# Optimization experiments

Hardware: AMD Instinct MI355X
Metric: run time of the kernel (lower is better)

The kernel has to match this reference:

```python
import jax, jax.numpy as jnp
from jax import lax
import numpy as np

V, D, H, E, L, B = 512, 128, 64, 4, 60, 4096
ADJ = 184  # ((180 + 7) // 8) * 8


def setup_inputs() -> dict:
    key = jax.random.key(0)
    it = iter(jax.random.split(key, 64))

    def nrm(shape, s=0.05):
        return jax.random.normal(next(it), shape, dtype=jnp.float32) * s

    x = jax.random.randint(next(it), (B, L), 0, V, dtype=jnp.int32)
    inp = {"x": x, "emb": nrm((V, D), 0.02).at[0].set(0.0)}  # padding_idx=0 row zero
    for d in ("f", "r"):
        inp[f"w_ih_{d}"] = nrm((4 * H, D)); inp[f"w_hh_{d}"] = nrm((4 * H, H))
        inp[f"b_ih_{d}"] = nrm((4 * H,)); inp[f"b_hh_{d}"] = nrm((4 * H,))
    for p, i_, h_, o_ in (("e", 1, 16, 8), ("l", 1, 16, 8), ("c", V, 32, 16), ("p", 6, 24, 12), ("x", 4, 16, 8)):
        inp[f"{p}_w1"] = nrm((h_, i_)); inp[f"{p}_b1"] = nrm((h_,))
        inp[f"{p}_w2"] = nrm((o_, h_)); inp[f"{p}_b2"] = nrm((o_,))
    inp["fp_w"] = nrm((ADJ, 180)); inp["fp_b"] = nrm((ADJ,))
    inp["attn_w"] = nrm((3 * ADJ, ADJ)); inp["attn_b"] = nrm((3 * ADJ,))
    inp["out_w"] = nrm((ADJ, ADJ)); inp["out_b"] = nrm((ADJ,))
    for i, (o_, i_) in enumerate(((128, ADJ), (64, 128), (32, 64), (E, 32)), 1):
        inp[f"g_w{i}"] = nrm((o_, i_)); inp[f"g_b{i}"] = nrm((o_,))
    return inp


def _mlp2(h, w1, b1, w2, b2):
    return jnp.maximum(h @ w1.T + b1, 0.0) @ w2.T + b2


def _lstm_final(xe, w_ih, w_hh, b_ih, b_hh):
    # torch LSTM gate order i, f, g, o; returns final hidden state [B, H]
    xg = jnp.einsum('bld,gd->blg', xe, w_ih) + b_ih
    h0 = jnp.zeros((xe.shape[0], H), xe.dtype)

    def step(carry, g_t):
        h, c = carry
        g = g_t + h @ w_hh.T + b_hh
        i, f, gg, o = jnp.split(g, 4, axis=-1)
        c = jax.nn.sigmoid(f) * c + jax.nn.sigmoid(i) * jnp.tanh(gg)
        h = jax.nn.sigmoid(o) * jnp.tanh(c)
        return (h, c), None

    (h, _), _ = lax.scan(step, (h0, h0), jnp.swapaxes(xg, 0, 1))
    return h


def _sequence_stats(x):
    # Fully vectorized equivalent of the per-sequence python loops
    f32 = jnp.float32
    mask = x != 0
    vlen = mask.sum(1)                                       # [B]
    vlenf = jnp.maximum(vlen, 1).astype(f32)
    pos = jnp.arange(L)
    # per-row histogram over valid tokens (torch.bincount of valid_seq)
    counts = jnp.zeros((B, V), f32).at[jnp.arange(B)[:, None], x].add(mask.astype(f32))
    probs = counts / jnp.maximum(counts.sum(1, keepdims=True), 1.0)
    entropy = -jnp.sum(probs * jnp.log(probs + 1e-8), axis=1)
    entropy = jnp.where(vlen > 1, entropy, 0.0)
    char_dist = counts / vlenf[:, None]
    # compact valid tokens to the front (torch: seq[seq != 0]), stable argsort
    order = jnp.argsort((~mask).astype(jnp.int32), axis=1)
    cseq = jnp.take_along_axis(x, order, axis=1)
    cseq = jnp.where(pos[None] < vlen[:, None], cseq, 0)
    a, b = cseq[:, :-1], cseq[:, 1:]
    pairmask = pos[: L - 1][None] < (vlen - 1)[:, None]
    den1 = jnp.maximum(vlen - 1, 1).astype(f32)
    repeat = ((a == b) & pairmask).sum(1) / den1
    inc = ((b > a) & pairmask).sum(1) / den1
    dec = ((b < a) & pairmask).sum(1) / den1
    m2 = pos[: L - 2][None] < (vlen - 2)[:, None]
    per = ((cseq[:, :-2] == cseq[:, 2:]) & m2).sum(1) / jnp.maximum(vlen - 2, 1)
    per = jnp.where(vlen >= 4, per, 0.0)
    diversity = (counts > 0).sum(1) / vlenf
    # longest run of equal consecutive tokens via cummax of reset positions
    eq = jnp.concatenate([jnp.zeros((B, 1), bool), (cseq[:, 1:] == cseq[:, :-1]) & (pos[1:][None] < vlen[:, None])], 1)
    lastreset = lax.cummax(jnp.where(eq, -1, pos[None]), axis=1)
    runlen = pos[None] - lastreset + 1
    max_rep = jnp.where(pos[None] < vlen[:, None], runlen, 0).max(1) / vlenf
    pattern = jnp.stack([repeat, inc, dec, per, diversity, max_rep], 1).astype(f32)
    pattern = jnp.where((vlen > 1)[:, None], pattern, 0.0)
    # unique bigrams: sort pair codes, count distinct valid codes
    codes = jnp.where(pairmask, a * V + b, -1)
    s = jnp.sort(codes, axis=1)
    prevc = jnp.concatenate([jnp.full((B, 1), -2, s.dtype), s[:, :-1]], 1)
    comp_ratio = ((s != prevc) & (s >= 0)).sum(1) / den1
    info_density = entropy / jnp.log(jnp.maximum(vlen, 2).astype(f32))
    # local complexity: mean over sliding windows of (#unique / w), w = min(5, len//2)
    wsel = jnp.minimum(5, vlen // 2)
    local = jnp.zeros((B,), f32)
    for w in (2, 3, 4, 5):
        nwin = L - w + 1
        sh = [cseq[:, k:k + nwin] for k in range(w)]
        u = jnp.ones((B, nwin), f32)
        for k in range(1, w):
            isnew = jnp.ones((B, nwin), bool)
            for m in range(k):
                isnew = isnew & (sh[k] != sh[m])
            u = u + isnew
        winmask = pos[:nwin][None] < (vlen - w + 1)[:, None]
        lc = (u * winmask).sum(1) / w / jnp.maximum(vlen - w + 1, 1)
        local = jnp.where(wsel == w, lc, local)
    trans = 1.0 - repeat  # transitions/(len-1) == 1 - repeat_ratio
    complexity = jnp.stack([comp_ratio, info_density, local, trans], 1).astype(f32)
    complexity = jnp.where((vlen > 1)[:, None], complexity, 0.0)
    return entropy, vlen, char_dist, pattern, complexity


def reference(x, emb, w_ih_f, w_hh_f, b_ih_f, b_hh_f, w_ih_r, w_hh_r, b_ih_r, b_hh_r, e_w1, e_b1, e_w2, e_b2, l_w1, l_b1, l_w2, l_b2, c_w1, c_b1, c_w2, c_b2, p_w1, p_b1, p_w2, p_b2, x_w1, x_b1, x_w2, x_b2, fp_w, fp_b, attn_w, attn_b, out_w, out_b, g_w1, g_b1, g_w2, g_b2, g_w3, g_b3, g_w4, g_b4):
    entropy, vlen, char_dist, pattern, complexity = _sequence_stats(x)
    xe = emb[x]                                               # [B, L, D]
    h_f = _lstm_final(xe, w_ih_f, w_hh_f, b_ih_f, b_hh_f)
    h_r = _lstm_final(xe[:, ::-1], w_ih_r, w_hh_r, b_ih_r, b_hh_r)
    feats = jnp.concatenate([
        h_f, h_r,
        _mlp2((entropy / 4.0)[:, None], e_w1, e_b1, e_w2, e_b2),
        _mlp2((vlen.astype(jnp.float32) / 60.0)[:, None], l_w1, l_b1, l_w2, l_b2),
        _mlp2(char_dist, c_w1, c_b1, c_w2, c_b2),
        _mlp2(pattern, p_w1, p_b1, p_w2, p_b2),
        _mlp2(complexity, x_w1, x_b1, x_w2, x_b2),
    ], axis=1)                                                # [B, 180]
    f = feats @ fp_w.T + fp_b                                 # [B, 184]
    # MultiheadAttention with seq_len == 1: softmax over a single key is 1,
    # so attended = out_proj(v_proj(f)) exactly (q/k projections cancel).
    wv, bv = attn_w[2 * ADJ:], attn_b[2 * ADJ:]
    attended = (f @ wv.T + bv) @ out_w.T + out_b
    h = jnp.maximum(attended @ g_w1.T + g_b1, 0.0)
    h = jnp.maximum(h @ g_w2.T + g_b2, 0.0)
    h = jnp.maximum(h @ g_w3.T + g_b3, 0.0)
    logits = h @ g_w4.T + g_b4
    return jax.nn.softmax(logits, axis=-1)  # eval path (training=False)
```

## Files before the change

### kernel.cpp

```cpp
#include <hip/hip_runtime.h>

#define BATCH 4096
#define SEQL  60
#define VOC   512
#define EMBD  128
#define HID   64
#define GATES 256
#define ADJ   184

typedef __attribute__((ext_vector_type(8))) short short8;
typedef __attribute__((ext_vector_type(4))) float f32x4;

__device__ __forceinline__ float sigm(float x) {
  return __builtin_amdgcn_rcpf(1.f + __expf(-x));
}
__device__ __forceinline__ float tanh_(float x) {
  float e = __expf(2.f * x);
  return 1.f - 2.f * __builtin_amdgcn_rcpf(e + 1.f);
}
__device__ __forceinline__ unsigned short f2bf(float f) {
  unsigned int u = __float_as_uint(f);
  unsigned int r = (u + 0x7fffu + ((u >> 16) & 1u)) >> 16;
  return (unsigned short)r;
}
__device__ __forceinline__ float dot4(float4 a, float4 b, float acc) {
  acc = fmaf(a.x, b.x, acc); acc = fmaf(a.y, b.y, acc);
  acc = fmaf(a.z, b.z, acc); acc = fmaf(a.w, b.w, acc);
  return acc;
}
__device__ __forceinline__ float wsumf(float v) {
  #pragma unroll
  for (int s = 32; s > 0; s >>= 1) v += __shfl_xor(v, s, 64);
  return v;
}
__device__ __forceinline__ int wsumi(int v) {
  #pragma unroll
  for (int s = 32; s > 0; s >>= 1) v += __shfl_xor(v, s, 64);
  return v;
}
__device__ __forceinline__ int wmaxi(int v) {
  #pragma unroll
  for (int s = 32; s > 0; s >>= 1) v = max(v, __shfl_xor(v, s, 64));
  return v;
}

__global__ __launch_bounds__(256) void k_mega(
    const int* __restrict__ x, const float* __restrict__ emb,
    const float* __restrict__ wih_f, const float* __restrict__ bif, const float* __restrict__ bhf,
    const float* __restrict__ wih_r, const float* __restrict__ bir, const float* __restrict__ bhr,
    const float* __restrict__ whh_f, const float* __restrict__ whh_r,
    const float* __restrict__ g_w1, const float* __restrict__ g_b1,
    const float* __restrict__ out_w, const float* __restrict__ out_b,
    const float* __restrict__ attn_w, const float* __restrict__ attn_b,
    const float* __restrict__ fp_w, const float* __restrict__ fp_b,
    const float* __restrict__ g_w2, const float* __restrict__ g_w3,
    const float* __restrict__ g_w4,
    float* __restrict__ ent_o, float* __restrict__ vlen_o,
    float* __restrict__ pat_o, float* __restrict__ cpx_o,
    unsigned int* __restrict__ cnt_o,
    float* __restrict__ G_f, float* __restrict__ G_r,
    unsigned short* __restrict__ Wfrag,
    float* __restrict__ A, float* __restrict__ avb,
    float* __restrict__ Bp, float* __restrict__ vb,
    float* __restrict__ g_w2t, float* __restrict__ g_w3t, float* __restrict__ g_w4t) {
  __shared__ unsigned int cnt[4][512];
  __shared__ unsigned short q[4][68];
  const int bid = blockIdx.x;
  const int tid = threadIdx.x;

  if (bid < 1024) {
    const int lane = tid & 63;
    const int wid = tid >> 6;
    const int row = bid * 4 + wid;
    unsigned int* cr = cnt[wid];
    unsigned short* qr = q[wid];

    for (int i = lane; i < 512; i += 64) cr[i] = 0u;
    qr[lane] = 0;
    if (lane < 4) qr[64 + lane] = 0;
    int v = (lane < 60) ? x[row * 60 + lane] : 0;
    bool act = (v != 0);
    unsigned long long amask = __ballot(act);
    int n = __popcll(amask);
    __syncthreads();
    if (act) {
      int pos = __popcll(amask & ((1ull << lane) - 1ull));
      qr[pos] = (unsigned short)v;
      atomicAdd(&cr[v], 1u);
    }
    __syncthreads();

    float vlenf = (float)(n >= 1 ? n : 1);
    float inv = 1.f / vlenf;

    float ent = 0.f; int distinct = 0;
    #pragma unroll
    for (int j = 0; j < 8; j++) {
      unsigned int c = cr[lane + j * 64];
      if (c) {
        distinct++;
        float p = (float)c * inv;
        ent -= p * __logf(p + 1e-8f);
      }
    }
    ent = wsumf(ent);
    distinct = wsumi(distinct);

    int a = qr[lane], b = qr[lane + 1], c2 = qr[lane + 2];
    bool v1 = (lane + 1 < n);
    bool v2 = (lane + 2 < n);
    int rep  = __popcll(__ballot(v1 && (a == b)));
    int incs = __popcll(__ballot(v1 && (b > a)));
    int decs = __popcll(__ballot(v1 && (b < a)));
    int per2 = __popcll(__ballot(v2 && (a == c2)));

    int prev = (lane > 0) ? (int)qr[lane - 1] : -1;
    bool isst = (lane < n) && (lane == 0 || a != prev);
    unsigned long long smask = __ballot(isst);
    int len = 0;
    if (isst) {
      unsigned long long hi = (lane < 63) ? (smask >> (lane + 1)) : 0ull;
      int next = hi ? (lane + __ffsll((unsigned long long)hi)) : n;
      len = next - lane;
    }
    int maxrun = wmaxi(len);

    int unique = 1;
    int lim = v1 ? lane : 0;
    for (int jj = 0; jj < lim; jj++) {
      if ((int)qr[jj] == a && (int)qr[jj + 1] == b) { unique = 0; break; }
    }
    int dc = __popcll(__ballot(v1 && unique));

    int wl = n >> 1; if (wl > 5) wl = 5;
    float local = 0.f;
    if (wl >= 2) {
      bool pv = (lane + wl <= n);
      int u = 0;
      if (pv) {
        int t0 = qr[lane], t1 = qr[lane + 1], t2 = qr[lane + 2];
        int t3 = qr[lane + 3], t4 = qr[lane + 4];
        u = 1;
        u += (t1 != t0);
        if (wl >= 3) u += (int)((t2 != t1) && (t2 != t0));
        if (wl >= 4) u += (int)((t3 != t2) && (t3 != t1) && (t3 != t0));
        if (wl >= 5) u += (int)((t4 != t3) && (t4 != t2) && (t4 != t1) && (t4 != t0));
      }
      int usum = wsumi(u);
      int denw = n - wl + 1; if (denw < 1) denw = 1;
      local = (float)usum / (float)wl / (float)denw;
    }

    float den1 = (float)((n - 1) >= 1 ? (n - 1) : 1);
    float repeat = (float)rep / den1;
    float per = (n >= 4) ? (float)per2 / (float)((n - 2) >= 1 ? (n - 2) : 1) : 0.f;
    float entz = (n > 1) ? ent : 0.f;
    float z = (n > 1) ? 1.f : 0.f;

    if (lane == 0) {
      ent_o[row] = entz;
      vlen_o[row] = (float)n;
      pat_o[row * 6 + 0] = repeat * z;
      pat_o[row * 6 + 1] = (float)incs / den1 * z;
      pat_o[row * 6 + 2] = (float)decs / den1 * z;
      pat_o[row * 6 + 3] = per * z;
      pat_o[row * 6 + 4] = (float)distinct * inv * z;
      pat_o[row * 6 + 5] = (float)maxrun * inv * z;
      cpx_o[row * 4 + 0] = (float)dc / den1 * z;
      cpx_o[row * 4 + 1] = entz / __logf((float)(n >= 2 ? n : 2)) * z;
      cpx_o[row * 4 + 2] = local * z;
      cpx_o[row * 4 + 3] = (1.f - repeat) * z;
    }
    for (int i = lane; i < 128; i += 64) {
      unsigned int p = cr[4 * i] | (cr[4 * i + 1] << 8) |
                       (cr[4 * i + 2] << 16) | (cr[4 * i + 3] << 24);
      cnt_o[row * 128 + i] = p;
    }
  } else if (bid < 1152) {
    const int bx = bid - 1024;
    const int dir = bx >> 6;
    const int rem = bx & 63;
    const int v0 = (rem >> 2) * 32;
    const int j0 = (rem & 3) * 64;
    const float* W = dir ? wih_r : wih_f;
    const float* bi = dir ? bir : bif;
    const float* bh = dir ? bhr : bhf;
    float* G = dir ? G_r : G_f;
    const int vp = tid >> 4;
    const int jq = tid & 15;
    const int v = v0 + vp * 2;
    const int j = j0 + jq * 4;
    const int gg = j >> 6;
    const int u0 = j & 63;

    const float4* E0 = (const float4*)(emb + (size_t)v * 128);
    const float4* E1 = (const float4*)(emb + (size_t)(v + 1) * 128);
    const float4* W0 = (const float4*)(W + (size_t)j * 128);
    const float4* W1 = (const float4*)(W + (size_t)(j + 1) * 128);
    const float4* W2 = (const float4*)(W + (size_t)(j + 2) * 128);
    const float4* W3 = (const float4*)(W + (size_t)(j + 3) * 128);

    float a00 = 0.f, a01 = 0.f, a02 = 0.f, a03 = 0.f;
    float a10 = 0.f, a11 = 0.f, a12 = 0.f, a13 = 0.f;
    #pragma unroll 4
    for (int d4 = 0; d4 < 32; d4++) {
      float4 e0 = E0[d4], e1 = E1[d4];
      float4 w0 = W0[d4], w1 = W1[d4], w2 = W2[d4], w3 = W3[d4];
      a00 = dot4(e0, w0, a00); a01 = dot4(e0, w1, a01);
      a02 = dot4(e0, w2, a02); a03 = dot4(e0, w3, a03);
      a10 = dot4(e1, w0, a10); a11 = dot4(e1, w1, a11);
      a12 = dot4(e1, w2, a12); a13 = dot4(e1, w3, a13);
    }
    float b0v = bi[j] + bh[j], b1v = bi[j + 1] + bh[j + 1];
    float b2v = bi[j + 2] + bh[j + 2], b3v = bi[j + 3] + bh[j + 3];
    float* g0 = G + (size_t)v * 256 + u0 * 4 + gg;
    g0[0]  = a00 + b0v; g0[4]  = a01 + b1v;
    g0[8]  = a02 + b2v; g0[12] = a03 + b3v;
    float* g1 = g0 + 256;
    g1[0]  = a10 + b0v; g1[4]  = a11 + b1v;
    g1[8]  = a12 + b2v; g1[12] = a13 + b3v;
  } else if (bid < 1280) {
    const int i = bid - 1152;
    const int j = tid;
    const float* g1r = g_w1 + (size_t)i * ADJ;
    if (j < ADJ) {
      float a0 = 0.f, a1 = 0.f, a2 = 0.f, a3 = 0.f;
      for (int k = 0; k < ADJ; k += 4) {
        a0 = fmaf(g1r[k],     out_w[(size_t)(k)     * ADJ + j], a0);
        a1 = fmaf(g1r[k + 1], out_w[(size_t)(k + 1) * ADJ + j], a1);
        a2 = fmaf(g1r[k + 2], out_w[(size_t)(k + 2) * ADJ + j], a2);
        a3 = fmaf(g1r[k + 3], out_w[(size_t)(k + 3) * ADJ + j], a3);
      }
      A[(size_t)i * ADJ + j] = (a0 + a1) + (a2 + a3);
    } else if (j == ADJ) {
      float a0 = 0.f;
      for (int k = 0; k < ADJ; k++) a0 = fmaf(g1r[k], out_b[k], a0);
      avb[i] = a0 + g_b1[i];
    }
  } else if (bid < 1464) {
    const int k = bid - 1280;
    const int j = tid;
    const float* wvr = attn_w + (size_t)(2 * ADJ + k) * ADJ;
    if (j < 180) {
      float a0 = 0.f, a1 = 0.f, a2 = 0.f, a3 = 0.f;
      for (int m = 0; m < ADJ; m += 4) {
        a0 = fmaf(wvr[m],     fp_w[(size_t)(m)     * 180 + j], a0);
        a1 = fmaf(wvr[m + 1], fp_w[(size_t)(m + 1) * 180 + j], a1);
        a2 = fmaf(wvr[m + 2], fp_w[(size_t)(m + 2) * 180 + j], a2);
        a3 = fmaf(wvr[m + 3], fp_w[(size_t)(m + 3) * 180 + j], a3);
      }
      Bp[(size_t)k * 180 + j] = (a0 + a1) + (a2 + a3);
    } else if (j == 180) {
      float a0 = 0.f;
      for (int m = 0; m < ADJ; m++) a0 = fmaf(wvr[m], fp_b[m], a0);
      vb[k] = a0 + attn_b[2 * ADJ + k];
    }
  } else if (bid < 1480) {
    const int id = (bid - 1464) * 256 + tid;
    const int lane = id & 63;
    const int fc = id >> 6;
    const int c = fc & 1;
    const int gg = (fc >> 1) & 3;
    const int w = (fc >> 3) & 3;
    const int dir = fc >> 5;
    const float* whh = dir ? whh_r : whh_f;
    const int n = gg * 64 + w * 16 + (lane & 15);
    const int kb = c * 32 + (lane >> 4) * 8;
    unsigned short* o = Wfrag + (size_t)id * 8;
    #pragma unroll
    for (int j = 0; j < 8; j++) o[j] = f2bf(whh[n * 64 + kb + j]);
  } else {
    for (int i = tid; i < 64 * 128; i += 256) {
      int o = i >> 7, k = i & 127;
      g_w2t[k * 64 + o] = g_w2[i];
    }
    for (int i = tid; i < 32 * 64; i += 256) {
      int o = i >> 6, k = i & 63;
      g_w3t[k * 32 + o] = g_w3[i];
    }
    if (tid < 128) {
      int o = tid >> 5, k = tid & 31;
      g_w4t[k * 4 + o] = g_w4[tid];
    }
  }
}

__global__ __launch_bounds__(192) void k_prep2(
    const float* __restrict__ A, const float* __restrict__ avb,
    const float* __restrict__ Bp, const float* __restrict__ vb,
    float* __restrict__ C1t, float* __restrict__ c1b) {
  const int i = blockIdx.x, j = threadIdx.x;
  const float* Ar = A + (size_t)i * ADJ;
  if (j < 180) {
    float a0 = 0.f, a1 = 0.f, a2 = 0.f, a3 = 0.f;
    for (int k = 0; k < ADJ; k += 4) {
      a0 = fmaf(Ar[k],     Bp[(size_t)(k)     * 180 + j], a0);
      a1 = fmaf(Ar[k + 1], Bp[(size_t)(k + 1) * 180 + j], a1);
      a2 = fmaf(Ar[k + 2], Bp[(size_t)(k + 2) * 180 + j], a2);
      a3 = fmaf(Ar[k + 3], Bp[(size_t)(k + 3) * 180 + j], a3);
    }
    C1t[(size_t)j * 128 + i] = (a0 + a1) + (a2 + a3);
  } else if (j == 180) {
    float a0 = 0.f;
    for (int k = 0; k < ADJ; k++) a0 = fmaf(Ar[k], vb[k], a0);
    c1b[i] = a0 + avb[i];
  }
}

#define LSTM_STEP(T, CUR, NXT)                                                 \
  {                                                                            \
    const unsigned short* hb = hbuf[(T) & 1];                                  \
    short8 a0 = *(const short8*)(hb + ln * 72 + kg * 8);                       \
    short8 a1 = *(const short8*)(hb + ln * 72 + 32 + kg * 8);                  \
    if ((T) < 59) {                                                            \
      int tsn = dir ? (58 - (T)) : ((T) + 1);                                  \
      unsigned long long tp =                                                  \
          *(const unsigned long long*)(tokp + tsn * 16 + kg * 4);              \
      int ta = (int)(tp & 0xffffull), tb = (int)((tp >> 16) & 0xffffull);      \
      int tc = (int)((tp >> 32) & 0xffffull), td = (int)(tp >> 48);            \
      NXT[0] = *(const float4*)(G + (size_t)ta * 256 + u4);                    \
      NXT[1] = *(const float4*)(G + (size_t)tb * 256 + u4);                    \
      NXT[2] = *(const float4*)(G + (size_t)tc * 256 + u4);                    \
      NXT[3] = *(const float4*)(G + (size_t)td * 256 + u4);                    \
    }                                                                          \
    f32x4 z0 = {0.f, 0.f, 0.f, 0.f};                                           \
    f32x4 acc0 = z0, acc1 = z0, acc2 = z0, acc3 = z0;                          \
    acc0 = __builtin_amdgcn_mfma_f32_16x16x32_bf16(a0, bfr[0][0], acc0, 0, 0, 0); \
    acc1 = __builtin_amdgcn_mfma_f32_16x16x32_bf16(a0, bfr[1][0], acc1, 0, 0, 0); \
    acc2 = __builtin_amdgcn_mfma_f32_16x16x32_bf16(a0, bfr[2][0], acc2, 0, 0, 0); \
    acc3 = __builtin_amdgcn_mfma_f32_16x16x32_bf16(a0, bfr[3][0], acc3, 0, 0, 0); \
    acc0 = __builtin_amdgcn_mfma_f32_16x16x32_bf16(a1, bfr[0][1], acc0, 0, 0, 0); \
    acc1 = __builtin_amdgcn_mfma_f32_16x16x32_bf16(a1, bfr[1][1], acc1, 0, 0, 0); \
    acc2 = __builtin_amdgcn_mfma_f32_16x16x32_bf16(a1, bfr[2][1], acc2, 0, 0, 0); \
    acc3 = __builtin_amdgcn_mfma_f32_16x16x32_bf16(a1, bfr[3][1], acc3, 0, 0, 0); \
    unsigned short* hw = hbuf[((T) + 1) & 1];                                  \
    _Pragma("unroll")                                                          \
    for (int r = 0; r < 4; r++) {                                              \
      float gi = acc0[r] + CUR[r].x;                                           \
      float gf = acc1[r] + CUR[r].y;                                           \
      float gc = acc2[r] + CUR[r].z;                                           \
      float go = acc3[r] + CUR[r].w;                                           \
      float cn = sigm(gf) * cst[r] + sigm(gi) * tanh_(gc);                     \
      cst[r] = cn;                                                             \
      float h = sigm(go) * tanh_(cn);                                          \
      hw[(kg * 4 + r) * 72 + u] = f2bf(h);                                     \
      if ((T) == 59) ho[(size_t)(b0 + kg * 4 + r) * 64 + u] = h;               \
    }                                                                          \
    __syncthreads();                                                           \
  }

__global__ __launch_bounds__(256) void k_lstm(
    const int* __restrict__ x,
    const float* __restrict__ G_f, const float* __restrict__ G_r,
    const unsigned short* __restrict__ Wfrag,
    float* __restrict__ hf_o, float* __restrict__ hr_o) {
  __shared__ __align__(16) unsigned short hbuf[2][16 * 72];
  __shared__ __align__(8) unsigned short tokp[60 * 16];
  const int tid = threadIdx.x;
  const int lane = tid & 63;
  const int w = tid >> 6;
  const int dir = blockIdx.x >> 8;
  const int blk = blockIdx.x & 255;
  const int b0 = blk << 4;
  const float* G = dir ? G_r : G_f;
  float* ho = dir ? hr_o : hf_o;

  for (int i = tid; i < 960; i += 256) {
    int r = i / 60, t = i - r * 60;
    tokp[t * 16 + r] = (unsigned short)x[(size_t)(b0 + r) * 60 + t];
  }
  for (int i = tid; i < 16 * 72; i += 256) hbuf[0][i] = 0;

  short8 bfr[4][2];
  #pragma unroll
  for (int gg = 0; gg < 4; gg++)
    #pragma unroll
    for (int c = 0; c < 2; c++) {
      int idx = (((dir * 4 + w) * 4 + gg) * 2 + c) * 64 + lane;
      bfr[gg][c] = *(const short8*)(Wfrag + (size_t)idx * 8);
    }

  const int kg = lane >> 4;
  const int ln = lane & 15;
  const int u = w * 16 + ln;
  const int u4 = u * 4;
  float cst[4] = {0.f, 0.f, 0.f, 0.f};
  float4 gvA[4], gvB[4];

  __syncthreads();

  {
    int ts0 = dir ? 59 : 0;
    unsigned long long tp =
        *(const unsigned long long*)(tokp + ts0 * 16 + kg * 4);
    int ta = (int)(tp & 0xffffull), tb = (int)((tp >> 16) & 0xffffull);
    int tc = (int)((tp >> 32) & 0xffffull), td = (int)(tp >> 48);
    gvA[0] = *(const float4*)(G + (size_t)ta * 256 + u4);
    gvA[1] = *(const float4*)(G + (size_t)tb * 256 + u4);
    gvA[2] = *(const float4*)(G + (size_t)tc * 256 + u4);
    gvA[3] = *(const float4*)(G + (size_t)td * 256 + u4);
  }

  #pragma unroll 1
  for (int tt = 0; tt < 30; tt++) {
    const int t0 = tt * 2, t1 = tt * 2 + 1;
    LSTM_STEP(t0, gvA, gvB)
    LSTM_STEP(t1, gvB, gvA)
  }
}

#define FSTR 192
#define CFS  520

__global__ __launch_bounds__(256) void k_head(
    const float* __restrict__ hf, const float* __restrict__ hr,
    const float* __restrict__ ent, const float* __restrict__ vlen,
    const float* __restrict__ pat, const float* __restrict__ cpx,
    const unsigned int* __restrict__ cnts,
    const float* __restrict__ e_w1, const float* __restrict__ e_b1,
    const float* __restrict__ e_w2, const float* __restrict__ e_b2,
    const float* __restrict__ l_w1, const float* __restrict__ l_b1,
    const float* __restrict__ l_w2, const float* __restrict__ l_b2,
    const float* __restrict__ c_w1, const float* __restrict__ c_b1,
    const float* __restrict__ c_w2, const float* __restrict__ c_b2,
    const float* __restrict__ p_w1, const float* __restrict__ p_b1,
    const float* __restrict__ p_w2, const float* __restrict__ p_b2,
    const float* __restrict__ x_w1, const float* __restrict__ x_b1,
    const float* __restrict__ x_w2, const float* __restrict__ x_b2,
    const float* __restrict__ C1t, const float* __restrict__ c1b,
    const float* __restrict__ g_w2t, const float* __restrict__ g_b2,
    const float* __restrict__ g_w3t, const float* __restrict__ g_b3,
    const float* __restrict__ g_w4t, const float* __restrict__ g_b4,
    float* __restrict__ out) {
  __shared__ float feat[8 * FSTR];
  __shared__ float cf[8 * CFS];
  __shared__ float h1[8 * 128];
  __shared__ float h2[8 * 64];
  __shared__ float h3[8 * 32];
  __shared__ float h1c[8 * 33];
  __shared__ float lg[32];
  const int tid = threadIdx.x;
  const int b0 = blockIdx.x * 8;

  if (tid < 128) {
    int r = tid >> 4, c = tid & 15;
    float4 vv = ((const float4*)(hf + (size_t)(b0 + r) * 64))[c];
    *(float4*)(feat + r * FSTR + c * 4) = vv;
  } else {
    int t = tid - 128;
    int r = t >> 4, c = t & 15;
    float4 vv = ((const float4*)(hr + (size_t)(b0 + r) * 64))[c];
    *(float4*)(feat + r * FSTR + 64 + c * 4) = vv;
  }
  {
    uint4 u4v = *(const uint4*)(cnts + (size_t)b0 * 128 + tid * 4);
    int r = tid >> 5, c0 = (tid & 31) * 16;
    float* dst = cf + r * CFS + c0;
    unsigned int uu[4] = {u4v.x, u4v.y, u4v.z, u4v.w};
    #pragma unroll
    for (int q = 0; q < 4; q++) {
      float4 f4;
      f4.x = (float)(uu[q] & 255u);
      f4.y = (float)((uu[q] >> 8) & 255u);
      f4.z = (float)((uu[q] >> 16) & 255u);
      f4.w = (float)(uu[q] >> 24);
      *(float4*)(dst + q * 4) = f4;
    }
  }
  __syncthreads();
  {
    int o = tid >> 3, r = tid & 7;
    const float4* Wc = (const float4*)(c_w1 + (size_t)o * 512);
    const float4* cv = (const float4*)(cf + r * CFS);
    float a0 = 0.f, a1 = 0.f;
    #pragma unroll 4
    for (int k4 = 0; k4 < 128; k4 += 2) {
      a0 = dot4(Wc[k4], cv[k4], a0);
      a1 = dot4(Wc[k4 + 1], cv[k4 + 1], a1);
    }
    float invv = __builtin_amdgcn_rcpf(fmaxf(vlen[b0 + r], 1.f));
    h1c[r * 33 + o] = fmaxf((a0 + a1) * invv + c_b1[o], 0.f);
  }
  __syncthreads();
  if (tid < 32) {
    const int m = tid & 3, r = tid >> 2, b = b0 + r;
    float tt[24];
    if (m == 0) {
      float ein = ent[b] * 0.25f;
      #pragma unroll
      for (int o = 0; o < 16; o++) tt[o] = fmaxf(e_w1[o] * ein + e_b1[o], 0.f);
      #pragma unroll
      for (int o = 0; o < 8; o++) {
        float a = e_b2[o];
        #pragma unroll
        for (int k = 0; k < 16; k++) a = fmaf(e_w2[o * 16 + k], tt[k], a);
        feat[r * FSTR + 128 + o] = a;
      }
    } else if (m == 1) {
      float lin = vlen[b] * (1.f / 60.f);
      #pragma unroll
      for (int o = 0; o < 16; o++) tt[o] = fmaxf(l_w1[o] * lin + l_b1[o], 0.f);
      #pragma unroll
      for (int o = 0; o < 8; o++) {
        float a = l_b2[o];
        #pragma unroll
        for (int k = 0; k < 16; k++) a = fmaf(l_w2[o * 16 + k], tt[k], a);
        feat[r * FSTR + 136 + o] = a;
      }
    } else if (m == 2) {
      float pin[6];
      #pragma unroll
      for (int k = 0; k < 6; k++) pin[k] = pat[b * 6 + k];
      #pragma unroll
      for (int o = 0; o < 24; o++) {
        float a = p_b1[o];
        #pragma unroll
        for (int k = 0; k < 6; k++) a = fmaf(p_w1[o * 6 + k], pin[k], a);
        tt[o] = fmaxf(a, 0.f);
      }
      #pragma unroll
      for (int o = 0; o < 12; o++) {
        float a = p_b2[o];
        #pragma unroll
        for (int k = 0; k < 24; k++) a = fmaf(p_w2[o * 24 + k], tt[k], a);
        feat[r * FSTR + 160 + o] = a;
      }
    } else {
      float xin[4];
      #pragma unroll
      for (int k = 0; k < 4; k++) xin[k] = cpx[b * 4 + k];
      #pragma unroll
      for (int o = 0; o < 16; o++) {
        float a = x_b1[o];
        #pragma unroll
        for (int k = 0; k < 4; k++) a = fmaf(x_w1[o * 4 + k], xin[k], a);
        tt[o] = fmaxf(a, 0.f);
      }
      #pragma unroll
      for (int o = 0; o < 8; o++) {
        float a = x_b2[o];
        #pragma unroll
        for (int k = 0; k < 16; k++) a = fmaf(x_w2[o * 16 + k], tt[k], a);
        feat[r * FSTR + 172 + o] = a;
      }
    }
  } else if (tid >= 64 && tid < 192) {
    int t = tid - 64;
    int r = t >> 4, o = t & 15;
    float a = c_b2[o];
    const float* hh = h1c + r * 33;
    #pragma unroll
    for (int k = 0; k < 32; k++) a = fmaf(c_w2[o * 32 + k], hh[k], a);
    feat[r * FSTR + 144 + o] = a;
  }
  __syncthreads();

  {
    const int o = tid & 127, rg = tid >> 7;
    const float* f0p = feat + (rg * 4 + 0) * FSTR;
    const float* f1p = feat + (rg * 4 + 1) * FSTR;
    const float* f2p = feat + (rg * 4 + 2) * FSTR;
    const float* f3p = feat + (rg * 4 + 3) * FSTR;
    float a0 = 0.f, a1 = 0.f, a2 = 0.f, a3 = 0.f;
    #pragma unroll 3
    for (int k4 = 0; k4 < 45; k4++) {
      float w0 = C1t[(size_t)(k4 * 4 + 0) * 128 + o];
      float w1 = C1t[(size_t)(k4 * 4 + 1) * 128 + o];
      float w2 = C1t[(size_t)(k4 * 4 + 2) * 128 + o];
      float w3 = C1t[(size_t)(k4 * 4 + 3) * 128 + o];
      float4 f0 = *(const float4*)(f0p + k4 * 4);
      float4 f1 = *(const float4*)(f1p + k4 * 4);
      float4 f2 = *(const float4*)(f2p + k4 * 4);
      float4 f3 = *(const float4*)(f3p + k4 * 4);
      a0 = fmaf(w0, f0.x, a0); a0 = fmaf(w1, f0.y, a0);
      a0 = fmaf(w2, f0.z, a0); a0 = fmaf(w3, f0.w, a0);
      a1 = fmaf(w0, f1.x, a1); a1 = fmaf(w1, f1.y, a1);
      a1 = fmaf(w2, f1.z, a1); a1 = fmaf(w3, f1.w, a1);
      a2 = fmaf(w0, f2.x, a2); a2 = fmaf(w1, f2.y, a2);
      a2 = fmaf(w2, f2.z, a2); a2 = fmaf(w3, f2.w, a2);
      a3 = fmaf(w0, f3.x, a3); a3 = fmaf(w1, f3.y, a3);
      a3 = fmaf(w2, f3.z, a3); a3 = fmaf(w3, f3.w, a3);
    }
    float bb = c1b[o];
    h1[(rg * 4 + 0) * 128 + o] = fmaxf(a0 + bb, 0.f);
    h1[(rg * 4 + 1) * 128 + o] = fmaxf(a1 + bb, 0.f);
    h1[(rg * 4 + 2) * 128 + o] = fmaxf(a2 + bb, 0.f);
    h1[(rg * 4 + 3) * 128 + o] = fmaxf(a3 + bb, 0.f);
  }
  __syncthreads();
  {
    const int o = tid & 63, rg = tid >> 6;
    const float* f0p = h1 + (rg * 2 + 0) * 128;
    const float* f1p = h1 + (rg * 2 + 1) * 128;
    float a0 = 0.f, a1 = 0.f;
    #pragma unroll 4
    for (int k4 = 0; k4 < 32; k4++) {
      float w0 = g_w2t[(k4 * 4 + 0) * 64 + o];
      float w1 = g_w2t[(k4 * 4 + 1) * 64 + o];
      float w2 = g_w2t[(k4 * 4 + 2) * 64 + o];
      float w3 = g_w2t[(k4 * 4 + 3) * 64 + o];
      float4 f0 = *(const float4*)(f0p + k4 * 4);
      float4 f1 = *(const float4*)(f1p + k4 * 4);
      a0 = fmaf(w0, f0.x, a0); a0 = fmaf(w1, f0.y, a0);
      a0 = fmaf(w2, f0.z, a0); a0 = fmaf(w3, f0.w, a0);
      a1 = fmaf(w0, f1.x, a1); a1 = fmaf(w1, f1.y, a1);
      a1 = fmaf(w2, f1.z, a1); a1 = fmaf(w3, f1.w, a1);
    }
    float bb = g_b2[o];
    h2[(rg * 2 + 0) * 64 + o] = fmaxf(a0 + bb, 0.f);
    h2[(rg * 2 + 1) * 64 + o] = fmaxf(a1 + bb, 0.f);
  }
  __syncthreads();
  {
    const int o = tid & 31, rg = tid >> 5;
    const float* fp = h2 + rg * 64;
    float a = 0.f;
    #pragma unroll 4
    for (int k4 = 0; k4 < 16; k4++) {
      float w0 = g_w3t[(k4 * 4 + 0) * 32 + o];
      float w1 = g_w3t[(k4 * 4 + 1) * 32 + o];
      float w2 = g_w3t[(k4 * 4 + 2) * 32 + o];
      float w3 = g_w3t[(k4 * 4 + 3) * 32 + o];
      float4 f0 = *(const float4*)(fp + k4 * 4);
      a = fmaf(w0, f0.x, a); a = fmaf(w1, f0.y, a);
      a = fmaf(w2, f0.z, a); a = fmaf(w3, f0.w, a);
    }
    h3[rg * 32 + o] = fmaxf(a + g_b3[o], 0.f);
  }
  __syncthreads();
  if (tid < 32) {
    int r = tid >> 2, o = tid & 3;
    const float* hh = h3 + r * 32;
    float a = g_b4[o];
    #pragma unroll
    for (int k = 0; k < 32; k++) a = fmaf(g_w4t[k * 4 + o], hh[k], a);
    lg[tid] = a;
  }
  __syncthreads();
  if (tid < 8) {
    float l0 = lg[tid * 4 + 0], l1 = lg[tid * 4 + 1];
    float l2 = lg[tid * 4 + 2], l3 = lg[tid * 4 + 3];
    float m = fmaxf(fmaxf(l0, l1), fmaxf(l2, l3));
    float e0 = __expf(l0 - m), e1 = __expf(l1 - m);
    float e2 = __expf(l2 - m), e3 = __expf(l3 - m);
    float is = __builtin_amdgcn_rcpf(e0 + e1 + e2 + e3);
    float4 o4; o4.x = e0 * is; o4.y = e1 * is; o4.z = e2 * is; o4.w = e3 * is;
    *(float4*)(out + (size_t)(b0 + tid) * 4) = o4;
  }
}

extern "C" void kernel_launch(void* const* d_in, const int* in_sizes, int n_in,
                              void* d_out, int out_size, void* d_ws, size_t ws_size,
                              hipStream_t stream) {
  const int*   x     = (const int*)d_in[0];
  const float* emb   = (const float*)d_in[1];
  const float* wih_f = (const float*)d_in[2];
  const float* whh_f = (const float*)d_in[3];
  const float* bih_f = (const float*)d_in[4];
  const float* bhh_f = (const float*)d_in[5];
  const float* wih_r = (const float*)d_in[6];
  const float* whh_r = (const float*)d_in[7];
  const float* bih_r = (const float*)d_in[8];
  const float* bhh_r = (const float*)d_in[9];
  const float* e_w1 = (const float*)d_in[10]; const float* e_b1 = (const float*)d_in[11];
  const float* e_w2 = (const float*)d_in[12]; const float* e_b2 = (const float*)d_in[13];
  const float* l_w1 = (const float*)d_in[14]; const float* l_b1 = (const float*)d_in[15];
  const float* l_w2 = (const float*)d_in[16]; const float* l_b2 = (const float*)d_in[17];
  const float* c_w1 = (const float*)d_in[18]; const float* c_b1 = (const float*)d_in[19];
  const float* c_w2 = (const float*)d_in[20]; const float* c_b2 = (const float*)d_in[21];
  const float* p_w1 = (const float*)d_in[22]; const float* p_b1 = (const float*)d_in[23];
  const float* p_w2 = (const float*)d_in[24]; const float* p_b2 = (const float*)d_in[25];
  const float* x_w1 = (const float*)d_in[26]; const float* x_b1 = (const float*)d_in[27];
  const float* x_w2 = (const float*)d_in[28]; const float* x_b2 = (const float*)d_in[29];
  const float* fp_w = (const float*)d_in[30]; const float* fp_b = (const float*)d_in[31];
  const float* attn_w = (const float*)d_in[32]; const float* attn_b = (const float*)d_in[33];
  const float* out_w = (const float*)d_in[34]; const float* out_b = (const float*)d_in[35];
  const float* g_w1 = (const float*)d_in[36]; const float* g_b1 = (const float*)d_in[37];
  const float* g_w2 = (const float*)d_in[38]; const float* g_b2 = (const float*)d_in[39];
  const float* g_w3 = (const float*)d_in[40]; const float* g_b3 = (const float*)d_in[41];
  const float* g_w4 = (const float*)d_in[42]; const float* g_b4 = (const float*)d_in[43];

  float* ws   = (float*)d_ws;
  float* G_f  = ws;
  float* G_r  = G_f  + 512 * 256;
  float* hfw  = G_r  + 512 * 256;
  float* hrw  = hfw  + BATCH * 64;
  float* entw = hrw  + BATCH * 64;
  float* vlnw = entw + BATCH;
  float* patw = vlnw + BATCH;
  float* cpxw = patw + BATCH * 6;
  unsigned int* cntw = (unsigned int*)(cpxw + BATCH * 4);
  float* Aw   = (float*)(cntw + BATCH * 128);
  float* avbw = Aw + 128 * ADJ;
  float* Bpw  = avbw + 128;
  float* vbw  = Bpw + ADJ * 180;
  float* C1t  = vbw + ADJ;
  float* c1b  = C1t + 180 * 128;
  float* g2t  = c1b + 128;
  float* g3t  = g2t + 128 * 64;
  float* g4t  = g3t + 64 * 32;
  unsigned short* Wfrag = (unsigned short*)(g4t + 32 * 4);

  k_mega<<<dim3(1481), dim3(256), 0, stream>>>(
      x, emb, wih_f, bih_f, bhh_f, wih_r, bih_r, bhh_r, whh_f, whh_r,
      g_w1, g_b1, out_w, out_b, attn_w, attn_b, fp_w, fp_b,
      g_w2, g_w3, g_w4,
      entw, vlnw, patw, cpxw, cntw, G_f, G_r, Wfrag,
      Aw, avbw, Bpw, vbw, g2t, g3t, g4t);
  k_prep2<<<dim3(128), dim3(192), 0, stream>>>(Aw, avbw, Bpw, vbw, C1t, c1b);
  k_lstm<<<dim3(512), dim3(256), 0, stream>>>(x, G_f, G_r, Wfrag, hfw, hrw);
  k_head<<<dim3(BATCH / 8), dim3(256), 0, stream>>>(
      hfw, hrw, entw, vlnw, patw, cpxw, cntw,
      e_w1, e_b1, e_w2, e_b2, l_w1, l_b1, l_w2, l_b2,
      c_w1, c_b1, c_w2, c_b2, p_w1, p_b1, p_w2, p_b2,
      x_w1, x_b1, x_w2, x_b2, C1t, c1b,
      g2t, g_b2, g3t, g_b3, g4t, g_b4,
      (float*)d_out);
}
```

Baseline: 277.4 us.

## Fold prep2 into LSTM launch, shuffle-based bigram uniqueness, transpose c_w1, byte-offset gathers

Removes the separate k_prep2 launch by running its 128 blocks as extra blocks in the LSTM kernel, which saves one launch and overlaps that work with the recurrence. The bigram distinct-count check now compares values across lanes with wave shuffles instead of a per-lane LDS scan with early exit. It also pre-transposes c_w1 in the setup kernel so the head kernel reads the weights coalesced, and stores token indices as precomputed byte offsets to simplify the gather address math in the LSTM. The extra blocks appended to the LSTM grid could delay the tail, and the shuffle loop always runs 58 iterations.

```diff
diff --git a/kernel.cpp b/kernel.cpp
--- a/kernel.cpp
+++ b/kernel.cpp
@@ -54,7 +54,7 @@
     const float* __restrict__ attn_w, const float* __restrict__ attn_b,
     const float* __restrict__ fp_w, const float* __restrict__ fp_b,
     const float* __restrict__ g_w2, const float* __restrict__ g_w3,
-    const float* __restrict__ g_w4,
+    const float* __restrict__ g_w4, const float* __restrict__ c_w1,
     float* __restrict__ ent_o, float* __restrict__ vlen_o,
     float* __restrict__ pat_o, float* __restrict__ cpx_o,
     unsigned int* __restrict__ cnt_o,
@@ -62,7 +62,8 @@
     unsigned short* __restrict__ Wfrag,
     float* __restrict__ A, float* __restrict__ avb,
     float* __restrict__ Bp, float* __restrict__ vb,
-    float* __restrict__ g_w2t, float* __restrict__ g_w3t, float* __restrict__ g_w4t) {
+    float* __restrict__ g_w2t, float* __restrict__ g_w3t, float* __restrict__ g_w4t,
+    float* __restrict__ c_w1t) {
   __shared__ unsigned int cnt[4][512];
   __shared__ unsigned short q[4][68];
   const int bid = blockIdx.x;
@@ -125,12 +126,14 @@
     }
     int maxrun = wmaxi(len);
 
-    int unique = 1;
-    int lim = v1 ? lane : 0;
-    for (int jj = 0; jj < lim; jj++) {
-      if ((int)qr[jj] == a && (int)qr[jj + 1] == b) { unique = 0; break; }
-    }
-    int dc = __popcll(__ballot(v1 && unique));
+    int code = v1 ? (a * VOC + b) : -1;
+    int unique = v1 ? 1 : 0;
+    #pragma unroll 1
+    for (int j = 0; j < 58; j++) {
+      int cj = __shfl(code, j, 64);
+      if (j < lane && cj == code) unique = 0;
+    }
+    int dc = __popcll(__ballot(unique != 0));
 
     int wl = n >> 1; if (wl > 5) wl = 5;
     float local = 0.f;
@@ -269,7 +272,7 @@
     unsigned short* o = Wfrag + (size_t)id * 8;
     #pragma unroll
     for (int j = 0; j < 8; j++) o[j] = f2bf(whh[n * 64 + kb + j]);
-  } else {
+  } else if (bid == 1480) {
     for (int i = tid; i < 64 * 128; i += 256) {
       int o = i >> 7, k = i & 127;
       g_w2t[k * 64 + o] = g_w2[i];
@@ -282,28 +285,13 @@
       int o = tid >> 5, k = tid & 31;
       g_w4t[k * 4 + o] = g_w4[tid];
     }
-  }
-}
-
-__global__ __launch_bounds__(192) void k_prep2(
-    const float* __restrict__ A, const float* __restrict__ avb,
-    const float* __restrict__ Bp, const float* __restrict__ vb,
-    float* __restrict__ C1t, float* __restrict__ c1b) {
-  const int i = blockIdx.x, j = threadIdx.x;
-  const float* Ar = A + (size_t)i * ADJ;
-  if (j < 180) {
-    float a0 = 0.f, a1 = 0.f, a2 = 0.f, a3 = 0.f;
-    for (int k = 0; k < ADJ; k += 4) {
-      a0 = fmaf(Ar[k],     Bp[(size_t)(k)     * 180 + j], a0);
-      a1 = fmaf(Ar[k + 1], Bp[(size_t)(k + 1) * 180 + j], a1);
-      a2 = fmaf(Ar[k + 2], Bp[(size_t)(k + 2) * 180 + j], a2);
-      a3 = fmaf(Ar[k + 3], Bp[(size_t)(k + 3) * 180 + j], a3);
-    }
-    C1t[(size_t)j * 128 + i] = (a0 + a1) + (a2 + a3);
-  } else if (j == 180) {
-    float a0 = 0.f;
-    for (int k = 0; k < ADJ; k++) a0 = fmaf(Ar[k], vb[k], a0);
-    c1b[i] = a0 + avb[i];
+  } else {
+    const int base = (bid - 1481) * 2048;
+    for (int i = tid; i < 2048; i += 256) {
+      int idx = base + i;
+      int o = idx >> 9, k = idx & 511;
+      c_w1t[k * 32 + o] = c_w1[idx];
+    }
   }
 }
 
@@ -314,14 +302,11 @@
     short8 a1 = *(const short8*)(hb + ln * 72 + 32 + kg * 8);                  \
     if ((T) < 59) {                                                            \
       int tsn = dir ? (58 - (T)) : ((T) + 1);                                  \
-      unsigned long long tp =                                                  \
-          *(const unsigned long long*)(tokp + tsn * 16 + kg * 4);              \
-      int ta = (int)(tp & 0xffffull), tb = (int)((tp >> 16) & 0xffffull);      \
-      int tc = (int)((tp >> 32) & 0xffffull), td = (int)(tp >> 48);            \
-      NXT[0] = *(const float4*)(G + (size_t)ta * 256 + u4);                    \
-      NXT[1] = *(const float4*)(G + (size_t)tb * 256 + u4);                    \
-      NXT[2] = *(const float4*)(G + (size_t)tc * 256 + u4);                    \
-      NXT[3] = *(const float4*)(G + (size_t)td * 256 + u4);                    \
+      uint4 of4 = *(const uint4*)(tokoff + tsn * 16 + kg * 4);                 \
+      NXT[0] = *(const float4*)(Gb + of4.x + ub);                              \
+      NXT[1] = *(const float4*)(Gb + of4.y + ub);                              \
+      NXT[2] = *(const float4*)(Gb + of4.z + ub);                              \
+      NXT[3] = *(const float4*)(Gb + of4.w + ub);                              \
     }                                                                          \
     f32x4 z0 = {0.f, 0.f, 0.f, 0.f};                                           \
     f32x4 acc0 = z0, acc1 = z0, acc2 = z0, acc3 = z0;                          \
@@ -353,21 +338,46 @@
     const int* __restrict__ x,
     const float* __restrict__ G_f, const float* __restrict__ G_r,
     const unsigned short* __restrict__ Wfrag,
+    const float* __restrict__ A, const float* __restrict__ avb,
+    const float* __restrict__ Bp, const float* __restrict__ vb,
+    float* __restrict__ C1t, float* __restrict__ c1b,
     float* __restrict__ hf_o, float* __restrict__ hr_o) {
   __shared__ __align__(16) unsigned short hbuf[2][16 * 72];
-  __shared__ __align__(8) unsigned short tokp[60 * 16];
+  __shared__ __align__(16) unsigned int tokoff[60 * 16];
   const int tid = threadIdx.x;
+
+  if (blockIdx.x >= 512) {
+    const int i = blockIdx.x - 512, j = tid;
+    const float* Ar = A + (size_t)i * ADJ;
+    if (j < 180) {
+      float a0 = 0.f, a1 = 0.f, a2 = 0.f, a3 = 0.f;
+      for (int k = 0; k < ADJ; k += 4) {
+        a0 = fmaf(Ar[k],     Bp[(size_t)(k)     * 180 + j], a0);
+        a1 = fmaf(Ar[k + 1], Bp[(size_t)(k + 1) * 180 + j], a1);
+        a2 = fmaf(Ar[k + 2], Bp[(size_t)(k + 2) * 180 + j], a2);
+        a3 = fmaf(Ar[k + 3], Bp[(size_t)(k + 3) * 180 + j], a3);
+      }
+      C1t[(size_t)j * 128 + i] = (a0 + a1) + (a2 + a3);
+    } else if (j == 180) {
+      float a0 = 0.f;
+      for (int k = 0; k < ADJ; k++) a0 = fmaf(Ar[k], vb[k], a0);
+      c1b[i] = a0 + avb[i];
+    }
+    return;
+  }
+
   const int lane = tid & 63;
   const int w = tid >> 6;
   const int dir = blockIdx.x >> 8;
   const int blk = blockIdx.x & 255;
   const int b0 = blk << 4;
   const float* G = dir ? G_r : G_f;
+  const char* Gb = (const char*)G;
   float* ho = dir ? hr_o : hf_o;
 
   for (int i = tid; i < 960; i += 256) {
     int r = i / 60, t = i - r * 60;
-    tokp[t * 16 + r] = (unsigned short)x[(size_t)(b0 + r) * 60 + t];
+    tokoff[t * 16 + r] = ((unsigned int)x[(size_t)(b0 + r) * 60 + t]) << 10;
   }
   for (int i = tid; i < 16 * 72; i += 256) hbuf[0][i] = 0;
 
@@ -383,7 +393,7 @@
   const int kg = lane >> 4;
   const int ln = lane & 15;
   const int u = w * 16 + ln;
-  const int u4 = u * 4;
+  const unsigned int ub = (unsigned int)u * 16;
   float cst[4] = {0.f, 0.f, 0.f, 0.f};
   float4 gvA[4], gvB[4];
 
@@ -391,14 +401,11 @@
 
   {
     int ts0 = dir ? 59 : 0;
-    unsigned long long tp =
-        *(const unsigned long long*)(tokp + ts0 * 16 + kg * 4);
-    int ta = (int)(tp & 0xffffull), tb = (int)((tp >> 16) & 0xffffull);
-    int tc = (int)((tp >> 32) & 0xffffull), td = (int)(tp >> 48);
-    gvA[0] = *(const float4*)(G + (size_t)ta * 256 + u4);
-    gvA[1] = *(const float4*)(G + (size_t)tb * 256 + u4);
-    gvA[2] = *(const float4*)(G + (size_t)tc * 256 + u4);
-    gvA[3] = *(const float4*)(G + (size_t)td * 256 + u4);
+    uint4 of4 = *(const uint4*)(tokoff + ts0 * 16 + kg * 4);
+    gvA[0] = *(const float4*)(Gb + of4.x + ub);
+    gvA[1] = *(const float4*)(Gb + of4.y + ub);
+    gvA[2] = *(const float4*)(Gb + of4.z + ub);
+    gvA[3] = *(const float4*)(Gb + of4.w + ub);
   }
 
   #pragma unroll 1
@@ -421,7 +428,7 @@
     const float* __restrict__ e_w2, const float* __restrict__ e_b2,
     const float* __restrict__ l_w1, const float* __restrict__ l_b1,
     const float* __restrict__ l_w2, const float* __restrict__ l_b2,
-    const float* __restrict__ c_w1, const float* __restrict__ c_b1,
+    const float* __restrict__ c_w1t, const float* __restrict__ c_b1,
     const float* __restrict__ c_w2, const float* __restrict__ c_b2,
     const float* __restrict__ p_w1, const float* __restrict__ p_b1,
     const float* __restrict__ p_w2, const float* __restrict__ p_b2,
@@ -458,28 +465,30 @@
     float* dst = cf + r * CFS + c0;
     unsigned int uu[4] = {u4v.x, u4v.y, u4v.z, u4v.w};
     #pragma unroll
-    for (int q = 0; q < 4; q++) {
+    for (int qq = 0; qq < 4; qq++) {
       float4 f4;
-      f4.x = (float)(uu[q] & 255u);
-      f4.y = (float)((uu[q] >> 8) & 255u);
-      f4.z = (float)((uu[q] >> 16) & 255u);
-      f4.w = (float)(uu[q] >> 24);
-      *(float4*)(dst + q * 4) = f4;
+      f4.x = (float)(uu[qq] & 255u);
+      f4.y = (float)((uu[qq] >> 8) & 255u);
+      f4.z = (float)((uu[qq] >> 16) & 255u);
+      f4.w = (float)(uu[qq] >> 24);
+      *(float4*)(dst + qq * 4) = f4;
     }
   }
   __syncthreads();
   {
-    int o = tid >> 3, r = tid & 7;
-    const float4* Wc = (const float4*)(c_w1 + (size_t)o * 512);
-    const float4* cv = (const float4*)(cf + r * CFS);
-    float a0 = 0.f, a1 = 0.f;
+    int o = tid & 31, r = tid >> 5;
+    const float* cv = cf + r * CFS;
+    float a0 = 0.f, a1 = 0.f, a2 = 0.f, a3 = 0.f;
     #pragma unroll 4
-    for (int k4 = 0; k4 < 128; k4 += 2) {
-      a0 = dot4(Wc[k4], cv[k4], a0);
-      a1 = dot4(Wc[k4 + 1], cv[k4 + 1], a1);
+    for (int k = 0; k < 512; k += 4) {
+      float4 c4 = *(const float4*)(cv + k);
+      a0 = fmaf(c_w1t[(k + 0) * 32 + o], c4.x, a0);
+      a1 = fmaf(c_w1t[(k + 1) * 32 + o], c4.y, a1);
+      a2 = fmaf(c_w1t[(k + 2) * 32 + o], c4.z, a2);
+      a3 = fmaf(c_w1t[(k + 3) * 32 + o], c4.w, a3);
     }
     float invv = __builtin_amdgcn_rcpf(fmaxf(vlen[b0 + r], 1.f));
-    h1c[r * 33 + o] = fmaxf((a0 + a1) * invv + c_b1[o], 0.f);
+    h1c[r * 33 + o] = fmaxf(((a0 + a1) + (a2 + a3)) * invv + c_b1[o], 0.f);
   }
   __syncthreads();
   if (tid < 32) {
@@ -699,20 +708,21 @@
   float* g2t  = c1b + 128;
   float* g3t  = g2t + 128 * 64;
   float* g4t  = g3t + 64 * 32;
-  unsigned short* Wfrag = (unsigned short*)(g4t + 32 * 4);
-
-  k_mega<<<dim3(1481), dim3(256), 0, stream>>>(
+  float* cw1t = g4t + 32 * 4;
+  unsigned short* Wfrag = (unsigned short*)(cw1t + 512 * 32);
+
+  k_mega<<<dim3(1489), dim3(256), 0, stream>>>(
       x, emb, wih_f, bih_f, bhh_f, wih_r, bih_r, bhh_r, whh_f, whh_r,
       g_w1, g_b1, out_w, out_b, attn_w, attn_b, fp_w, fp_b,
-      g_w2, g_w3, g_w4,
+      g_w2, g_w3, g_w4, c_w1,
       entw, vlnw, patw, cpxw, cntw, G_f, G_r, Wfrag,
-      Aw, avbw, Bpw, vbw, g2t, g3t, g4t);
-  k_prep2<<<dim3(128), dim3(192), 0, stream>>>(Aw, avbw, Bpw, vbw, C1t, c1b);
-  k_lstm<<<dim3(512), dim3(256), 0, stream>>>(x, G_f, G_r, Wfrag, hfw, hrw);
+      Aw, avbw, Bpw, vbw, g2t, g3t, g4t, cw1t);
+  k_lstm<<<dim3(640), dim3(256), 0, stream>>>(
+      x, G_f, G_r, Wfrag, Aw, avbw, Bpw, vbw, C1t, c1b, hfw, hrw);
   k_head<<<dim3(BATCH / 8), dim3(256), 0, stream>>>(
       hfw, hrw, entw, vlnw, patw, cpxw, cntw,
       e_w1, e_b1, e_w2, e_b2, l_w1, l_b1, l_w2, l_b2,
-      c_w1, c_b1, c_w2, c_b2, p_w1, p_b1, p_w2, p_b2,
+      cw1t, c_b1, c_w2, c_b2, p_w1, p_b1, p_w2, p_b2,
       x_w1, x_b1, x_w2, x_b2, C1t, c1b,
       g2t, g_b2, g3t, g_b3, g4t, g_b4,
       (float*)d_out);
```

Result: faster. 260.4 us (-6.1%).
